# Kernel tuning notes

Hardware: AMD Instinct MI355X
Metric: run time of the kernel (lower is better)

Reference implementation:

```python
import jax, jax.numpy as jnp
import numpy as np

N = 50000      # nodes
E = 800000     # edges (avg degree 16)
C = 128        # hidden_channels
L = 3          # CGConv layers actually executed (forward uses layers[1:] of 4)
K = 10         # category_number
BN_EPS = 1e-5


def setup_inputs() -> dict:
    key = jax.random.key(0)
    ks = jax.random.split(key, 18)
    s = 0.05
    inp = {
        "x": jax.random.normal(ks[0], (N, 7), dtype=jnp.float32),
        "edge_index": jax.random.randint(ks[1], (2, E), 0, N, dtype=jnp.int64),
        "edge_attr": jax.random.normal(ks[2], (E, 6), dtype=jnp.float32),
        # node / edge encoders
        "node_W": jax.random.normal(ks[3], (C, 7), dtype=jnp.float32) * s,
        "node_b": jax.random.normal(ks[4], (C,), dtype=jnp.float32) * s,
        "edge_W": jax.random.normal(ks[5], (C, 6), dtype=jnp.float32) * s,
        "edge_b": jax.random.normal(ks[6], (C,), dtype=jnp.float32) * s,
        # CGConv layers (stacked over L): lin_f, lin_s take concat(x_i, x_j, e) of dim 3C
        "Wf": jax.random.normal(ks[7], (L, C, 3 * C), dtype=jnp.float32) * s,
        "bf": jax.random.normal(ks[8], (L, C), dtype=jnp.float32) * s,
        "Ws": jax.random.normal(ks[9], (L, C, 3 * C), dtype=jnp.float32) * s,
        "bs": jax.random.normal(ks[10], (L, C), dtype=jnp.float32) * s,
        # batch norm (eval-mode: running stats)
        "gamma": jnp.ones((L, C), dtype=jnp.float32),
        "beta": jnp.zeros((L, C), dtype=jnp.float32),
        "bn_mean": jax.random.normal(ks[11], (L, C), dtype=jnp.float32) * s,
        "bn_var": jax.random.uniform(ks[12], (L, C), dtype=jnp.float32) + 0.5,
        # classifier head
        "lin_W": jax.random.normal(ks[13], (K, C), dtype=jnp.float32) * s,
        "lin_b": jax.random.normal(ks[14], (K,), dtype=jnp.float32) * s,
    }
    return inp


def _gcn_forward(x, edge_index, edge_attr, node_W, node_b, edge_W, edge_b,
                 Wf, bf, Ws, bs, gamma, beta, bn_mean, bn_var, lin_W, lin_b):
    h = x @ node_W.T + node_b                      # [N, C]
    e = edge_attr @ edge_W.T + edge_b              # [E, C]
    src = edge_index[0]                            # x_j (source)
    dst = edge_index[1]                            # x_i (target / aggregation index)
    n = h.shape[0]
    c = h.shape[1]
    for l in range(Wf.shape[0]):
        # split concat weight: z = [x_i | x_j | e]; W z = Wi x_i + Wj x_j + We e
        Wfi, Wfj, Wfe = Wf[l, :, :c], Wf[l, :, c:2 * c], Wf[l, :, 2 * c:]
        Wsi, Wsj, Wse = Ws[l, :, :c], Ws[l, :, c:2 * c], Ws[l, :, 2 * c:]
        # node-side projections once per node, then gather per edge
        hf_i, hf_j = h @ Wfi.T, h @ Wfj.T          # [N, C]
        hs_i, hs_j = h @ Wsi.T, h @ Wsj.T
        zf = hf_i[dst] + hf_j[src] + e @ Wfe.T + bf[l]   # [E, C]
        zs = hs_i[dst] + hs_j[src] + e @ Wse.T + bs[l]
        msg = jax.nn.sigmoid(zf) * jax.nn.softplus(zs)   # CGConv gated message
        agg = jax.ops.segment_max(msg, dst, num_segments=n)  # max aggregation
        agg = jnp.where(jnp.isneginf(agg), 0.0, agg)     # nodes with no in-edges -> 0
        # batch norm (eval) on aggregated messages
        agg = (agg - bn_mean[l]) * jax.lax.rsqrt(bn_var[l] + BN_EPS) * gamma[l] + beta[l]
        h = h + agg                                       # CGConv residual
    return h @ lin_W.T + lin_b, h


def reference(x, edge_index, edge_attr, node_W, node_b, edge_W, edge_b,
              Wf, bf, Ws, bs, gamma, beta, bn_mean, bn_var, lin_W, lin_b):
    return _gcn_forward(x, edge_index, edge_attr, node_W, node_b, edge_W, edge_b,
                        Wf, bf, Ws, bs, gamma, beta, bn_mean, bn_var, lin_W, lin_b)
```

## Files before the change

kernel.cpp:

```cpp
#include <hip/hip_runtime.h>

#define N_NODES 50000
#define N_EDGES 800000
#define C 128
#define NLAYERS 3
#define KOUT 10
#define BN_EPS 1e-5f
#define NGROUP_PAD 3128
#define SBLK 196
#define LOG2E 1.4426950408889634f
#define LN2   0.6931471805599453f

#if __has_builtin(__builtin_amdgcn_exp2f)
#define EXP2(x) __builtin_amdgcn_exp2f(x)
#else
#define EXP2(x) exp2f(x)
#endif
#if __has_builtin(__builtin_amdgcn_logf)
#define LOG2(x) __builtin_amdgcn_logf(x)
#else
#define LOG2(x) log2f(x)
#endif
#if __has_builtin(__builtin_amdgcn_rcpf)
#define RCP(x) __builtin_amdgcn_rcpf(x)
#else
#define RCP(x) (1.f / (x))
#endif

typedef float v2f __attribute__((ext_vector_type(2)));
typedef __attribute__((ext_vector_type(4))) float f32x4;
typedef __attribute__((ext_vector_type(8))) short s16x8;

__device__ __forceinline__ float bf2f(unsigned short u) {
    return __uint_as_float(((unsigned int)u) << 16);
}
__device__ __forceinline__ unsigned short f2bf(float f) {
    unsigned int b = __float_as_uint(f);
    b += 0x7fff + ((b >> 16) & 1);
    return (unsigned short)(b >> 16);
}
__device__ __forceinline__ float blo(unsigned int u) { return __uint_as_float(u << 16); }
__device__ __forceinline__ float bhi(unsigned int u) { return __uint_as_float(u & 0xffff0000u); }
__device__ __forceinline__ unsigned int pk2bf(float lo, float hi) {
    return (unsigned int)f2bf(lo) | ((unsigned int)f2bf(hi) << 16);
}
__device__ __forceinline__ float loadf(const void* p, long long i, int bf) {
    return bf ? bf2f(((const unsigned short*)p)[i]) : ((const float*)p)[i];
}
__device__ __forceinline__ int loadi(const void* p, long long i, int i64) {
    return i64 ? (int)((const long long*)p)[i] : ((const int*)p)[i];
}

__device__ __forceinline__ int h16f_off(int n, int chunk) {
    int g = n >> 4, rr = n & 15;
    int ks = chunk >> 2, kq = chunk & 3;
    return (((g * 4 + ks) * 64) + kq * 16 + rr) * 8;
}
__device__ __forceinline__ int perm_o(int o) {
    int g = o >> 7, c = o & 127;
    return ((g & 2) ? 256 : 0) + ((c >> 2) << 3) + ((g & 1) ? 4 : 0) + (c & 3);
}

__global__ __launch_bounds__(256) void setup_kernel(
    int* __restrict__ deg, const unsigned int* __restrict__ gbits,
    const unsigned int* __restrict__ ebits, int* __restrict__ flags) {
    int b = blockIdx.x, t = threadIdx.x;
    if (b < SBLK) {
        int i = b * 256 + t;
        if (i <= N_NODES) deg[i] = 0;
    } else {
        __shared__ int nz;
        if (t == 0) nz = 0;
        __syncthreads();
        if (t < 63 && ebits[t * 2 + 1] != 0u) atomicAdd(&nz, 1);
        __syncthreads();
        if (t == 0) {
            flags[0] = (gbits[0] == 0x3F803F80u) ? 1 : 0;
            flags[1] = (nz == 0) ? 1 : 0;
        }
    }
}

__global__ __launch_bounds__(256) void work1_kernel(
    const void* __restrict__ edge_index, int* __restrict__ deg,
    const void* __restrict__ x, const void* __restrict__ node_W,
    const void* __restrict__ node_b, float* __restrict__ h,
    unsigned short* __restrict__ h16f,
    const void* __restrict__ Wf, const void* __restrict__ Ws,
    const void* __restrict__ bfv, const void* __restrict__ bsv,
    const void* __restrict__ edge_W, const void* __restrict__ edge_b,
    const void* __restrict__ gamma, const void* __restrict__ beta,
    const void* __restrict__ bn_mean, const void* __restrict__ bn_var,
    const void* __restrict__ lin_W, const void* __restrict__ lin_b,
    unsigned short* __restrict__ W2, float* __restrict__ Wfold,
    float* __restrict__ bfold,
    float* __restrict__ bnA, float* __restrict__ bnB,
    float* __restrict__ linWf, float* __restrict__ linbf,
    const int* __restrict__ flags) {
    int f = flags[0];
    int b = blockIdx.x, t = threadIdx.x;
    if (b < 3125) {
        int i64 = flags[1];
        int e = b * 256 + t;
        int dst = loadi(edge_index, (long long)N_EDGES + e, i64);
        atomicAdd(&deg[dst], 1);
    } else if (b < 3125 + 6250) {
        int gtid = (b - 3125) * 256 + t;
        int n = gtid >> 5;
        if (n >= N_NODES) return;
        int q = gtid & 31, c0 = q * 4;
        float xv[7];
#pragma unroll
        for (int j = 0; j < 7; ++j) xv[j] = loadf(x, (long long)n * 7 + j, f);
        float4 acc;
        float* ap = (float*)&acc;
#pragma unroll
        for (int i = 0; i < 4; ++i) {
            int c = c0 + i;
            float a = loadf(node_b, c, f);
#pragma unroll
            for (int j = 0; j < 7; ++j)
                a = fmaf(xv[j], loadf(node_W, (long long)c * 7 + j, f), a);
            ap[i] = a;
        }
        ((float4*)h)[(long long)n * 32 + q] = acc;
        ushort4 s;
        s.x = f2bf(ap[0]); s.y = f2bf(ap[1]); s.z = f2bf(ap[2]); s.w = f2bf(ap[3]);
        *((ushort4*)(h16f + h16f_off(n, q >> 1) + (q & 1) * 4)) = s;
    } else {
        int bb = b - 9375;
        if (bb < 768) {
            int idx = bb * 256 + t;
            int k = idx & 127;
            int o = (idx >> 7) & 511;
            int l = idx >> 16;
            int c = o & 127;
            int g = o >> 7;
            long long base = (long long)l * C * 3 * C + (long long)c * 3 * C;
            float v;
            if (g == 0)      v = loadf(Wf, base + k, f);
            else if (g == 1) v = loadf(Ws, base + k, f);
            else if (g == 2) v = loadf(Wf, base + C + k, f);
            else             v = loadf(Ws, base + C + k, f);
            v *= LOG2E;
            int p = perm_o(o);
            int rt = p >> 4, rr = p & 15;
            int ch = k >> 3, j = k & 7;
            int ks = ch >> 2, kq = ch & 3;
            size_t w2i = ((((size_t)l * 32 + rt) * 4 + ks) * 64 + kq * 16 + rr) * 8 + j;
            W2[w2i] = f2bf(v);
        } else if (bb < 774) {
            if (t >= 128) return;
            int cc = bb - 768;
            int l = cc >> 1, s = cc & 1;
            const void* W = s ? Ws : Wf;
            const void* bias = s ? bsv : bfv;
            long long wbase = (long long)l * C * 3 * C + (long long)t * 3 * C + 2 * C;
            float acc[6] = {0.f, 0.f, 0.f, 0.f, 0.f, 0.f};
            float bacc = 0.f;
            for (int k = 0; k < C; ++k) {
                float w = loadf(W, wbase + k, f);
#pragma unroll
                for (int j = 0; j < 6; ++j)
                    acc[j] = fmaf(w, loadf(edge_W, k * 6 + j, f), acc[j]);
                bacc = fmaf(w, loadf(edge_b, k, f), bacc);
            }
#pragma unroll
            for (int j = 0; j < 6; ++j) Wfold[cc * 768 + j * C + t] = acc[j] * LOG2E;
            bfold[cc * C + t] = (bacc + loadf(bias, l * C + t, f)) * LOG2E;
        } else if (bb < 779) {
            int idx = (bb - 774) * 256 + t;
            if (idx < KOUT * C) linWf[idx] = loadf(lin_W, idx, f);
            if (idx < KOUT) linbf[idx] = loadf(lin_b, idx, f);
        } else {
            int idx = (bb - 779) * 256 + t;
            if (idx < NLAYERS * C) {
                float mn = loadf(bn_mean, idx, f);
                float vr = loadf(bn_var, idx, f);
                float gm = loadf(gamma, idx, f);
                float bt = loadf(beta, idx, f);
                float a = gm * rsqrtf(vr + BN_EPS);
                bnA[idx] = a * LN2;
                bnB[idx] = bt - mn * a;
            }
        }
    }
}

__global__ __launch_bounds__(256) void scan1_kernel(
    const int* __restrict__ deg, int* __restrict__ bsum) {
    __shared__ int ws[4];
    int i = blockIdx.x * 256 + threadIdx.x;
    int v = (i < N_NODES) ? deg[i] : 0;
#pragma unroll
    for (int o = 32; o >= 1; o >>= 1) v += __shfl_down(v, o);
    if ((threadIdx.x & 63) == 0) ws[threadIdx.x >> 6] = v;
    __syncthreads();
    if (threadIdx.x == 0) bsum[blockIdx.x] = ws[0] + ws[1] + ws[2] + ws[3];
}

__global__ __launch_bounds__(256) void scan2_kernel(int* __restrict__ bsum) {
    __shared__ int ls[256];
    int t = threadIdx.x;
    int v = (t < SBLK) ? bsum[t] : 0;
    ls[t] = v;
    __syncthreads();
    for (int o = 1; o < 256; o <<= 1) {
        int u = (t >= o) ? ls[t - o] : 0;
        __syncthreads();
        ls[t] += u;
        __syncthreads();
    }
    bsum[t] = ls[t] - v;
}

__global__ __launch_bounds__(256) void scan3_kernel(
    const int* __restrict__ deg, const int* __restrict__ bsum,
    int* __restrict__ row, int* __restrict__ cursor) {
    __shared__ int ls[256];
    int t = threadIdx.x;
    int i = blockIdx.x * 256 + t;
    int v = (i < N_NODES) ? deg[i] : 0;
    ls[t] = v;
    __syncthreads();
    for (int o = 1; o < 256; o <<= 1) {
        int u = (t >= o) ? ls[t - o] : 0;
        __syncthreads();
        ls[t] += u;
        __syncthreads();
    }
    int excl = bsum[blockIdx.x] + ls[t] - v;
    if (i <= N_NODES) row[i] = excl;
    if (i < N_NODES) cursor[i] = excl;
}

__global__ __launch_bounds__(256) void scatter_kernel(
    const void* __restrict__ edge_index, const void* __restrict__ edge_attr,
    int* __restrict__ cursor, float* __restrict__ eatt,
    const int* __restrict__ flags) {
    int f = flags[0], i64 = flags[1];
    int e = blockIdx.x * blockDim.x + threadIdx.x;
    if (e >= N_EDGES) return;
    int src = loadi(edge_index, e, i64);
    int dst = loadi(edge_index, (long long)N_EDGES + e, i64);
    int pos = atomicAdd(&cursor[dst], 1);
    uint4 E;
    if (f) {
        const unsigned short* ea = (const unsigned short*)edge_attr;
        unsigned int b0 = ea[e * 6 + 0], b1 = ea[e * 6 + 1], b2 = ea[e * 6 + 2];
        unsigned int b3 = ea[e * 6 + 3], b4 = ea[e * 6 + 4], b5 = ea[e * 6 + 5];
        E.x = b0 | (b1 << 16); E.y = b2 | (b3 << 16); E.z = b4 | (b5 << 16);
    } else {
        const float* ea = (const float*)edge_attr;
        E.x = pk2bf(ea[e * 6 + 0], ea[e * 6 + 1]);
        E.y = pk2bf(ea[e * 6 + 2], ea[e * 6 + 3]);
        E.z = pk2bf(ea[e * 6 + 4], ea[e * 6 + 5]);
    }
    E.w = (unsigned int)src;
    ((uint4*)eatt)[pos] = E;
}

__global__ __launch_bounds__(256) void gemm_kernel(
    const unsigned short* __restrict__ h16f,
    const unsigned short* __restrict__ W2,
    unsigned short* __restrict__ hcat) {
    __shared__ float smem[4 * 16 * 66];
    float* ls = smem;
    int wid = threadIdx.x >> 6, lane = threadIdx.x & 63;
    int mtile = blockIdx.x >> 1;
    int n0 = (blockIdx.x & 1) * 256 + wid * 64;
    int m0 = mtile * 64, g0 = mtile * 4;
    int rt0 = n0 >> 4;
    int cw = lane & 15, kq = lane >> 4, rw = kq * 4;
    const s16x8* Ap = (const s16x8*)h16f;
    const s16x8* Bp = (const s16x8*)W2;
    f32x4 acc[4][4];
#pragma unroll
    for (int i = 0; i < 4; ++i)
#pragma unroll
        for (int j = 0; j < 4; ++j) acc[i][j] = (f32x4){0.f, 0.f, 0.f, 0.f};
#pragma unroll
    for (int ks = 0; ks < 4; ++ks) {
        s16x8 a[4], b[4];
#pragma unroll
        for (int mt = 0; mt < 4; ++mt)
            a[mt] = Ap[((g0 + mt) * 4 + ks) * 64 + lane];
#pragma unroll
        for (int nt = 0; nt < 4; ++nt)
            b[nt] = Bp[((rt0 + nt) * 4 + ks) * 64 + lane];
#pragma unroll
        for (int mt = 0; mt < 4; ++mt)
#pragma unroll
            for (int nt = 0; nt < 4; ++nt)
                acc[mt][nt] = __builtin_amdgcn_mfma_f32_16x16x32_bf16(
                    a[mt], b[nt], acc[mt][nt], 0, 0, 0);
    }
    float* lw = ls + wid * (16 * 66);
    int er = lane >> 2, ecg = lane & 3;
#pragma unroll
    for (int mt = 0; mt < 4; ++mt) {
#pragma unroll
        for (int nt = 0; nt < 4; ++nt)
#pragma unroll
            for (int reg = 0; reg < 4; ++reg)
                lw[(rw + reg) * 66 + nt * 16 + cw] = acc[mt][nt][reg];
        int m = m0 + mt * 16 + er;
        float vv[16];
#pragma unroll
        for (int t2 = 0; t2 < 8; ++t2) {
            float2 w = *((float2*)&lw[er * 66 + ecg * 16 + t2 * 2]);
            vv[t2 * 2] = w.x; vv[t2 * 2 + 1] = w.y;
        }
        if (m < N_NODES) {
            ushort4 u0, u1, u2, u3;
            u0.x=f2bf(vv[0]);  u0.y=f2bf(vv[1]);  u0.z=f2bf(vv[2]);  u0.w=f2bf(vv[3]);
            u1.x=f2bf(vv[4]);  u1.y=f2bf(vv[5]);  u1.z=f2bf(vv[6]);  u1.w=f2bf(vv[7]);
            u2.x=f2bf(vv[8]);  u2.y=f2bf(vv[9]);  u2.z=f2bf(vv[10]); u2.w=f2bf(vv[11]);
            u3.x=f2bf(vv[12]); u3.y=f2bf(vv[13]); u3.z=f2bf(vv[14]); u3.w=f2bf(vv[15]);
            ushort4* dst = (ushort4*)(hcat + (size_t)m * 512 + n0 + ecg * 16);
            dst[0] = u0; dst[1] = u1; dst[2] = u2; dst[3] = u3;
        }
    }
}

__global__ __launch_bounds__(64) void agg_kernel(
    const float* __restrict__ eatt,
    const int* __restrict__ row, const unsigned short* __restrict__ hcat,
    const float* __restrict__ Wfold, const float* __restrict__ bfold,
    float* __restrict__ h, unsigned short* __restrict__ h16f,
    const float* __restrict__ bnA, const float* __restrict__ bnB,
    void* __restrict__ outp,
    int layer, const int* __restrict__ flags) {
    int f = flags[0];
    int n = blockIdx.x;
    int lane = threadIdx.x & 63;
    int half = lane >> 5;
    int q = lane & 31;
    int c0 = q * 4;

    float4 bA = *((const float4*)(bnA + layer * C + c0));
    float4 bB = *((const float4*)(bnB + layer * C + c0));
    int r0 = row[n], r1 = row[n + 1];
    float mf[4] = {0.f, 0.f, 0.f, 0.f};

    const float* wfp = Wfold + (2 * layer + 0) * 768;
    const float* wsp = Wfold + (2 * layer + 1) * 768;
    v2f wf2[6][2], ws2[6][2];
#pragma unroll
    for (int j = 0; j < 6; ++j) {
        float4 a = *((const float4*)(wfp + j * C + c0));
        float4 b = *((const float4*)(wsp + j * C + c0));
        wf2[j][0] = (v2f){a.x, a.y}; wf2[j][1] = (v2f){a.z, a.w};
        ws2[j][0] = (v2f){b.x, b.y}; ws2[j][1] = (v2f){b.z, b.w};
    }
    float4 bfv = *((const float4*)(bfold + (2 * layer + 0) * C + c0));
    float4 bsv = *((const float4*)(bfold + (2 * layer + 1) * C + c0));
    uint4 ib = ((const uint4*)hcat)[(long long)n * 64 + q];
    v2f bf0 = (v2f){blo(ib.x) + bfv.x, bhi(ib.x) + bfv.y};
    v2f bf1 = (v2f){blo(ib.y) + bfv.z, bhi(ib.y) + bfv.w};
    v2f bs0 = (v2f){blo(ib.z) + bsv.x, bhi(ib.z) + bsv.y};
    v2f bs1 = (v2f){blo(ib.w) + bsv.z, bhi(ib.w) + bsv.w};

    auto body = [&](v2f hf0, v2f hf1, v2f hs0, v2f hs1, const float* ea) {
        v2f vf0 = bf0 + hf0, vf1 = bf1 + hf1;
        v2f vs0 = bs0 + hs0, vs1 = bs1 + hs1;
#pragma unroll
        for (int j = 0; j < 6; ++j) {
            v2f ej = (v2f){ea[j], ea[j]};
            vf0 = __builtin_elementwise_fma(ej, wf2[j][0], vf0);
            vf1 = __builtin_elementwise_fma(ej, wf2[j][1], vf1);
            vs0 = __builtin_elementwise_fma(ej, ws2[j][0], vs0);
            vs1 = __builtin_elementwise_fma(ej, ws2[j][1], vs1);
        }
        float zf[4] = {vf0.x, vf0.y, vf1.x, vf1.y};
        float zs[4] = {vs0.x, vs0.y, vs1.x, vs1.y};
#pragma unroll
        for (int i = 0; i < 4; ++i) {
            float sg = RCP(1.f + EXP2(-zf[i]));
            float sp = fmaxf(zs[i], 0.f) + LOG2(1.f + EXP2(-fabsf(zs[i])));
            mf[i] = fmaxf(mf[i], sg * sp);
        }
    };

    const uint4* hb = (const uint4*)hcat;
    const uint4* ep = (const uint4*)eatt;
    for (int p = r0 + half; p < r1; p += 2) {
        uint4 E = ep[p];
        uint4 jb = hb[(long long)E.w * 64 + 32 + q];
        float ea[6] = {blo(E.x), bhi(E.x), blo(E.y), bhi(E.y), blo(E.z), bhi(E.z)};
        body((v2f){blo(jb.x), bhi(jb.x)}, (v2f){blo(jb.y), bhi(jb.y)},
             (v2f){blo(jb.z), bhi(jb.z)}, (v2f){blo(jb.w), bhi(jb.w)}, ea);
    }
#pragma unroll
    for (int i = 0; i < 4; ++i) mf[i] = fmaxf(mf[i], __shfl_xor(mf[i], 32));

    if (half == 0) {
        float4 hv = ((float4*)h)[(long long)n * 32 + q];
        float* hp = (float*)&hv;
        const float* bAp = (const float*)&bA;
        const float* bBp = (const float*)&bB;
#pragma unroll
        for (int i = 0; i < 4; ++i)
            hp[i] += mf[i] * bAp[i] + bBp[i];
        ((float4*)h)[(long long)n * 32 + q] = hv;
        {
            ushort4 s;
            s.x = f2bf(hp[0]); s.y = f2bf(hp[1]); s.z = f2bf(hp[2]); s.w = f2bf(hp[3]);
            *((ushort4*)(h16f + h16f_off(n, q >> 1) + (q & 1) * 4)) = s;
        }
        if (layer == NLAYERS - 1) {
            if (f) {
                ushort4 s;
                s.x = f2bf(hp[0]); s.y = f2bf(hp[1]); s.z = f2bf(hp[2]); s.w = f2bf(hp[3]);
                *((ushort4*)((unsigned short*)outp + N_NODES * KOUT + n * C + c0)) = s;
            } else {
                *((float4*)((float*)outp + N_NODES * KOUT + n * C + c0)) = hv;
            }
        }
    }
}

__global__ __launch_bounds__(256) void out_kernel(
    const float* __restrict__ h, const float* __restrict__ linWf,
    const float* __restrict__ linbf, void* __restrict__ out,
    const int* __restrict__ flags) {
    int f = flags[0];
    int g = blockIdx.x * 16 + (threadIdx.x >> 4);
    int l16 = threadIdx.x & 15;
    if (g >= N_NODES) return;
    const float4* hr = (const float4*)(h + (long long)g * C) + l16 * 2;
    float4 a0 = hr[0], a1 = hr[1];
    float res = 0.f;
#pragma unroll
    for (int k = 0; k < KOUT; ++k) {
        const float4* wr = (const float4*)(linWf + (long long)k * C) + l16 * 2;
        float4 w0 = wr[0], w1 = wr[1];
        float p = a0.x * w0.x + a0.y * w0.y + a0.z * w0.z + a0.w * w0.w
                + a1.x * w1.x + a1.y * w1.y + a1.z * w1.z + a1.w * w1.w;
        p += __shfl_xor(p, 1); p += __shfl_xor(p, 2);
        p += __shfl_xor(p, 4); p += __shfl_xor(p, 8);
        if (l16 == k) res = p + linbf[k];
    }
    if (l16 < KOUT) {
        long long idx = (long long)g * KOUT + l16;
        if (f) ((unsigned short*)out)[idx] = f2bf(res);
        else   ((float*)out)[idx] = res;
    }
}

extern "C" void kernel_launch(void* const* d_in, const int* in_sizes, int n_in,
                              void* d_out, int out_size, void* d_ws, size_t ws_size,
                              hipStream_t stream) {
    const void* x          = d_in[0];
    const void* edge_index = d_in[1];
    const void* edge_attr  = d_in[2];
    const void* node_W     = d_in[3];
    const void* node_b     = d_in[4];
    const void* edge_W     = d_in[5];
    const void* edge_b     = d_in[6];
    const void* Wf         = d_in[7];
    const void* bf         = d_in[8];
    const void* Ws         = d_in[9];
    const void* bs         = d_in[10];
    const void* gamma      = d_in[11];
    const void* beta       = d_in[12];
    const void* bn_mean    = d_in[13];
    const void* bn_var     = d_in[14];
    const void* lin_W      = d_in[15];
    const void* lin_b      = d_in[16];

    const size_t sz_h    = (size_t)N_NODES * C * 4;
    const size_t sz_h16f = (size_t)NGROUP_PAD * 4 * 64 * 8 * 2;
    const size_t sz_hc16 = (size_t)N_NODES * 512 * 2;
    const size_t sz_w2   = (size_t)NLAYERS * 512 * C * 2;
    const size_t sz_eatt = (size_t)N_EDGES * 16;

    char* wsp = (char*)d_ws;
    size_t off = 0;
    auto alloc = [&](size_t bytes) -> void* {
        void* p = wsp + off; off += (bytes + 255) & ~(size_t)255; return p;
    };
    float*          h      = (float*)alloc(sz_h);
    unsigned short* h16f   = (unsigned short*)alloc(sz_h16f);
    unsigned short* hcat   = (unsigned short*)alloc(sz_hc16);
    int*            deg    = (int*)alloc((size_t)(N_NODES + 1) * 4);
    int*            rowp   = (int*)alloc((size_t)(N_NODES + 1) * 4);
    int*            cursor = (int*)alloc((size_t)(N_NODES + 1) * 4);
    int*            bsum   = (int*)alloc(256 * 4);
    float*          eatt   = (float*)alloc(sz_eatt);
    unsigned short* W2     = (unsigned short*)alloc(sz_w2);
    float*          Wfold  = (float*)alloc(6 * 768 * 4);
    float*          bfold  = (float*)alloc(6 * C * 4);
    float*          bnA    = (float*)alloc(NLAYERS * C * 4);
    float*          bnB    = (float*)alloc(NLAYERS * C * 4);
    float*          linWf  = (float*)alloc(KOUT * C * 4);
    float*          linbf  = (float*)alloc(KOUT * 4);
    int*            flags  = (int*)alloc(256);

    setup_kernel<<<SBLK + 1, 256, 0, stream>>>(
        deg, (const unsigned int*)gamma, (const unsigned int*)edge_index, flags);
    work1_kernel<<<10156, 256, 0, stream>>>(
        edge_index, deg, x, node_W, node_b, h, h16f,
        Wf, Ws, bf, bs, edge_W, edge_b, gamma, beta, bn_mean, bn_var,
        lin_W, lin_b, W2, Wfold, bfold, bnA, bnB, linWf, linbf, flags);
    scan1_kernel<<<SBLK, 256, 0, stream>>>(deg, bsum);
    scan2_kernel<<<1, 256, 0, stream>>>(bsum);
    scan3_kernel<<<SBLK, 256, 0, stream>>>(deg, bsum, rowp, cursor);
    scatter_kernel<<<3125, 256, 0, stream>>>(
        edge_index, edge_attr, cursor, eatt, flags);

    for (int l = 0; l < NLAYERS; ++l) {
        gemm_kernel<<<1564, 256, 0, stream>>>(
            h16f, W2 + (size_t)l * 512 * C, hcat);
        agg_kernel<<<N_NODES, 64, 0, stream>>>(
            eatt, rowp, hcat, Wfold, bfold, h, h16f,
            bnA, bnB, d_out, l, flags);
    }
    out_kernel<<<(N_NODES + 15) / 16, 256, 0, stream>>>(
        h, linWf, linbf, d_out, flags);
}
```

Baseline: 672.1 us.

## Replicate degree and cursor counters to spread atomic contention

Degree counting and scatter cursors are split into 8 replicated arrays, chosen by block index, so atomics to the same destination node are spread across copies. The scans sum the replicas and give each replica its own sub-range of positions within the node's CSR segment. The edge-count blocks are also interleaved with the node-encoder blocks in work1 so the two kinds of work overlap on the GPU. The cost is more memory to zero and read (8x counters) and extra loads in the scan kernels.

```diff
diff --git a/kernel.cpp b/kernel.cpp
--- a/kernel.cpp
+++ b/kernel.cpp
@@ -8,6 +8,9 @@
 #define BN_EPS 1e-5f
 #define NGROUP_PAD 3128
 #define SBLK 196
+#define NPAD 50048
+#define NREP 8
+#define ZBLK 1564
 #define LOG2E 1.4426950408889634f
 #define LN2   0.6931471805599453f
 
@@ -62,12 +65,12 @@
 }
 
 __global__ __launch_bounds__(256) void setup_kernel(
-    int* __restrict__ deg, const unsigned int* __restrict__ gbits,
+    int* __restrict__ deg_r, const unsigned int* __restrict__ gbits,
     const unsigned int* __restrict__ ebits, int* __restrict__ flags) {
     int b = blockIdx.x, t = threadIdx.x;
-    if (b < SBLK) {
+    if (b < ZBLK) {
         int i = b * 256 + t;
-        if (i <= N_NODES) deg[i] = 0;
+        deg_r[i] = 0;
     } else {
         __shared__ int nz;
         if (t == 0) nz = 0;
@@ -82,7 +85,7 @@
 }
 
 __global__ __launch_bounds__(256) void work1_kernel(
-    const void* __restrict__ edge_index, int* __restrict__ deg,
+    const void* __restrict__ edge_index, int* __restrict__ deg_r,
     const void* __restrict__ x, const void* __restrict__ node_W,
     const void* __restrict__ node_b, float* __restrict__ h,
     unsigned short* __restrict__ h16f,
@@ -99,13 +102,17 @@
     const int* __restrict__ flags) {
     int f = flags[0];
     int b = blockIdx.x, t = threadIdx.x;
-    if (b < 3125) {
+    if ((b & 3) == 3) {
+        int eb = b >> 2;
         int i64 = flags[1];
-        int e = b * 256 + t;
+        int e = eb * 256 + t;
         int dst = loadi(edge_index, (long long)N_EDGES + e, i64);
-        atomicAdd(&deg[dst], 1);
-    } else if (b < 3125 + 6250) {
-        int gtid = (b - 3125) * 256 + t;
+        atomicAdd(&deg_r[(size_t)(eb & (NREP - 1)) * NPAD + dst], 1);
+        return;
+    }
+    int ob = (b >> 2) * 3 + (b & 3);
+    if (ob < 6250) {
+        int gtid = ob * 256 + t;
         int n = gtid >> 5;
         if (n >= N_NODES) return;
         int q = gtid & 31, c0 = q * 4;
@@ -127,8 +134,8 @@
         ushort4 s;
         s.x = f2bf(ap[0]); s.y = f2bf(ap[1]); s.z = f2bf(ap[2]); s.w = f2bf(ap[3]);
         *((ushort4*)(h16f + h16f_off(n, q >> 1) + (q & 1) * 4)) = s;
-    } else {
-        int bb = b - 9375;
+    } else if (ob < 7031) {
+        int bb = ob - 6250;
         if (bb < 768) {
             int idx = bb * 256 + t;
             int k = idx & 127;
@@ -188,10 +195,14 @@
 }
 
 __global__ __launch_bounds__(256) void scan1_kernel(
-    const int* __restrict__ deg, int* __restrict__ bsum) {
+    const int* __restrict__ deg_r, int* __restrict__ bsum) {
     __shared__ int ws[4];
     int i = blockIdx.x * 256 + threadIdx.x;
-    int v = (i < N_NODES) ? deg[i] : 0;
+    int v = 0;
+    if (i < N_NODES) {
+#pragma unroll
+        for (int r = 0; r < NREP; ++r) v += deg_r[(size_t)r * NPAD + i];
+    }
 #pragma unroll
     for (int o = 32; o >= 1; o >>= 1) v += __shfl_down(v, o);
     if ((threadIdx.x & 63) == 0) ws[threadIdx.x >> 6] = v;
@@ -215,12 +226,20 @@
 }
 
 __global__ __launch_bounds__(256) void scan3_kernel(
-    const int* __restrict__ deg, const int* __restrict__ bsum,
-    int* __restrict__ row, int* __restrict__ cursor) {
+    const int* __restrict__ deg_r, const int* __restrict__ bsum,
+    int* __restrict__ row, int* __restrict__ cur_r) {
     __shared__ int ls[256];
     int t = threadIdx.x;
     int i = blockIdx.x * 256 + t;
-    int v = (i < N_NODES) ? deg[i] : 0;
+    int dr[NREP];
+    int v = 0;
+    if (i < N_NODES) {
+#pragma unroll
+        for (int r = 0; r < NREP; ++r) {
+            dr[r] = deg_r[(size_t)r * NPAD + i];
+            v += dr[r];
+        }
+    }
     ls[t] = v;
     __syncthreads();
     for (int o = 1; o < 256; o <<= 1) {
@@ -231,19 +250,26 @@
     }
     int excl = bsum[blockIdx.x] + ls[t] - v;
     if (i <= N_NODES) row[i] = excl;
-    if (i < N_NODES) cursor[i] = excl;
+    if (i < N_NODES) {
+        int c = excl;
+#pragma unroll
+        for (int r = 0; r < NREP; ++r) {
+            cur_r[(size_t)r * NPAD + i] = c;
+            c += dr[r];
+        }
+    }
 }
 
 __global__ __launch_bounds__(256) void scatter_kernel(
     const void* __restrict__ edge_index, const void* __restrict__ edge_attr,
-    int* __restrict__ cursor, float* __restrict__ eatt,
+    int* __restrict__ cur_r, float* __restrict__ eatt,
     const int* __restrict__ flags) {
     int f = flags[0], i64 = flags[1];
     int e = blockIdx.x * blockDim.x + threadIdx.x;
     if (e >= N_EDGES) return;
     int src = loadi(edge_index, e, i64);
     int dst = loadi(edge_index, (long long)N_EDGES + e, i64);
-    int pos = atomicAdd(&cursor[dst], 1);
+    int pos = atomicAdd(&cur_r[(size_t)(blockIdx.x & (NREP - 1)) * NPAD + dst], 1);
     uint4 E;
     if (f) {
         const unsigned short* ea = (const unsigned short*)edge_attr;
@@ -474,6 +500,7 @@
     const size_t sz_hc16 = (size_t)N_NODES * 512 * 2;
     const size_t sz_w2   = (size_t)NLAYERS * 512 * C * 2;
     const size_t sz_eatt = (size_t)N_EDGES * 16;
+    const size_t sz_rep  = (size_t)NREP * NPAD * 4;
 
     char* wsp = (char*)d_ws;
     size_t off = 0;
@@ -483,9 +510,9 @@
     float*          h      = (float*)alloc(sz_h);
     unsigned short* h16f   = (unsigned short*)alloc(sz_h16f);
     unsigned short* hcat   = (unsigned short*)alloc(sz_hc16);
-    int*            deg    = (int*)alloc((size_t)(N_NODES + 1) * 4);
+    int*            deg_r  = (int*)alloc(sz_rep);
     int*            rowp   = (int*)alloc((size_t)(N_NODES + 1) * 4);
-    int*            cursor = (int*)alloc((size_t)(N_NODES + 1) * 4);
+    int*            cur_r  = (int*)alloc(sz_rep);
     int*            bsum   = (int*)alloc(256 * 4);
     float*          eatt   = (float*)alloc(sz_eatt);
     unsigned short* W2     = (unsigned short*)alloc(sz_w2);
@@ -497,17 +524,17 @@
     float*          linbf  = (float*)alloc(KOUT * 4);
     int*            flags  = (int*)alloc(256);
 
-    setup_kernel<<<SBLK + 1, 256, 0, stream>>>(
-        deg, (const unsigned int*)gamma, (const unsigned int*)edge_index, flags);
-    work1_kernel<<<10156, 256, 0, stream>>>(
-        edge_index, deg, x, node_W, node_b, h, h16f,
+    setup_kernel<<<ZBLK + 1, 256, 0, stream>>>(
+        deg_r, (const unsigned int*)gamma, (const unsigned int*)edge_index, flags);
+    work1_kernel<<<12500, 256, 0, stream>>>(
+        edge_index, deg_r, x, node_W, node_b, h, h16f,
         Wf, Ws, bf, bs, edge_W, edge_b, gamma, beta, bn_mean, bn_var,
         lin_W, lin_b, W2, Wfold, bfold, bnA, bnB, linWf, linbf, flags);
-    scan1_kernel<<<SBLK, 256, 0, stream>>>(deg, bsum);
+    scan1_kernel<<<SBLK, 256, 0, stream>>>(deg_r, bsum);
     scan2_kernel<<<1, 256, 0, stream>>>(bsum);
-    scan3_kernel<<<SBLK, 256, 0, stream>>>(deg, bsum, rowp, cursor);
+    scan3_kernel<<<SBLK, 256, 0, stream>>>(deg_r, bsum, rowp, cur_r);
     scatter_kernel<<<3125, 256, 0, stream>>>(
-        edge_index, edge_attr, cursor, eatt, flags);
+        edge_index, edge_attr, cur_r, eatt, flags);
 
     for (int l = 0; l < NLAYERS; ++l) {
         gemm_kernel<<<1564, 256, 0, stream>>>(
```

New measurement: 652.8 us. 1.03x faster.
